# Kernel optimization log

Measured on AMD Instinct MI355X. Metric: run time of the kernel, lower is better.

The kernel has to match this reference:

```python
import jax, jax.numpy as jnp
import numpy as np

B, S, F, E, H, L = 16, 256, 512, 128, 64, 8


def _gru(x, Wih, Whh, bih, bhh):
    """torch-style GRU over time. x: [B,S,E] -> hidden states [B,S,H]."""
    xp = jnp.einsum('bse,ge->bsg', x, Wih) + bih  # [B,S,3H]

    def step(h, xt):
        gh = h @ Whh.T + bhh                      # [B,3H]
        xr, xz, xn = jnp.split(xt, 3, axis=-1)
        hr, hz, hn = jnp.split(gh, 3, axis=-1)
        r = jax.nn.sigmoid(xr + hr)
        z = jax.nn.sigmoid(xz + hz)
        n = jnp.tanh(xn + r * hn)
        h_new = (1.0 - z) * n + z * h
        return h_new, h_new

    h0 = jnp.zeros((x.shape[0], Whh.shape[1]), x.dtype)
    _, hs = jax.lax.scan(step, h0, jnp.swapaxes(xp, 0, 1))  # [S,B,H]
    return jnp.swapaxes(hs, 0, 1)


def setup_inputs() -> dict:
    ks = jax.random.split(jax.random.key(0), 24)
    u = lambda k, shape, n: jax.random.uniform(k, shape, jnp.float32, -1.0 / np.sqrt(n), 1.0 / np.sqrt(n))
    inp = {
        'X': jax.random.normal(ks[0], (B, S, F), jnp.float32),
        'M': jnp.ones((B, S), jnp.float32),
        'cur_M': jax.random.uniform(ks[1], (B, S), jnp.float32),
        # embed linear [E,F]
        'W_embed': u(ks[2], (E, F), F), 'b_embed': u(ks[3], (E,), F),
        # GRU alpha
        'Wih_a': u(ks[4], (3 * H, E), H), 'Whh_a': u(ks[5], (3 * H, H), H),
        'bih_a': u(ks[6], (3 * H,), H), 'bhh_a': u(ks[7], (3 * H,), H),
        # GRU beta
        'Wih_b': u(ks[8], (3 * H, E), H), 'Whh_b': u(ks[9], (3 * H, H), H),
        'bih_b': u(ks[10], (3 * H,), H), 'bhh_b': u(ks[11], (3 * H,), H),
        # attention linears
        'Wb': u(ks[12], (E, H), H), 'bb': u(ks[13], (E,), H),
        'Wa': u(ks[14], (1, H), H), 'ba': u(ks[15], (1,), H),
        # predict linear
        'Wp': u(ks[16], (L, E), E), 'bp': u(ks[17], (L,), E),
    }
    return inp


def reference(X, M, cur_M, W_embed, b_embed,
              Wih_a, Whh_a, bih_a, bhh_a,
              Wih_b, Whh_b, bih_b, bhh_b,
              Wb, bb, Wa, ba, Wp, bp):
    n_seq = X.shape[1]
    emb = jnp.einsum('bsf,ef->bse', X, W_embed) + b_embed          # [B,S,E]
    h_alpha = _gru(emb, Wih_a, Whh_a, bih_a, bhh_a)                # [B,S,H]
    h_beta = _gru(emb, Wih_b, Whh_b, bih_b, bhh_b)                 # [B,S,H]

    # RETAIN attention
    beta_w = jnp.tanh(jnp.einsum('bsh,eh->bse', h_beta, Wb) + bb)  # [B,S,E]
    corr = (jnp.einsum('bsh,oh->bso', h_alpha, Wa) + ba)[..., 0]   # [B,S]
    attn = jnp.exp(corr)                                           # [B,S] (indexed by j)
    flag = jnp.triu(jnp.ones((n_seq, n_seq), X.dtype))             # flag[i,j]=1 iff j>=i
    flag_m = flag[None, :, :] * M[:, None, :]                      # [B,S,S]
    num = attn[:, None, :] * flag_m                                # [B,i,j]
    denom = num.sum(-1, keepdims=True) + 1e-10                     # [B,S,1]
    alpha_w = num / denom                                          # [B,S,S]
    # sum_j alpha[b,i,j] * beta_w[b,j,:] * emb[b,j,:]  (same math as the
    # original broadcasted [B,S,S,E] product, without materializing it)
    weighted = jnp.einsum('bij,bje->bie', alpha_w, beta_w * emb)   # [B,S,E]

    all_output = (jnp.einsum('bse,le->bsl', weighted, Wp) + bp) * M[..., None]  # [B,S,L]
    cur_output = (all_output * cur_M[..., None]).sum(axis=1)                    # [B,L]
    return all_output, cur_output
```

## Files before the change

### kernel.cpp

```cpp
#include <hip/hip_runtime.h>
#include <math.h>

#define BB 16
#define SS 256
#define FF 512
#define EE 128
#define HH 64
#define GG 192
#define LL 8
#define TT 16

__device__ __forceinline__ float sigmoid_f(float x) {
    return 1.0f / (1.0f + __expf(-x));
}
__device__ __forceinline__ float tanh_f(float x) {
    return 1.0f - 2.0f / (1.0f + __expf(2.0f * x));
}

__device__ __forceinline__ void gemm_bt_body(
    const float* __restrict__ A, const float* __restrict__ Bm,
    const float* __restrict__ bias, float* __restrict__ C,
    int N, int K)
{
    __shared__ float As[32][68];
    __shared__ float Bs[64][68];
    const int t = threadIdx.x;
    const int row0 = blockIdx.x * 32;
    const int col0 = blockIdx.y * 64;
    const int tr = t & 7;
    const int tc = t >> 3;
    float acc[4][2] = {{0.f,0.f},{0.f,0.f},{0.f,0.f},{0.f,0.f}};

    for (int k0 = 0; k0 < K; k0 += 64) {
        {
            int r = t >> 3;
            int q = t & 7;
            const float* src = &A[(size_t)(row0 + r) * K + k0];
            #pragma unroll
            for (int it = 0; it < 2; ++it) {
                int kk = (q + it * 8) * 4;
                *(float4*)&As[r][kk] = *(const float4*)&src[kk];
            }
        }
        {
            int r = t >> 2;
            int q = t & 3;
            int n = col0 + r;
            #pragma unroll
            for (int it = 0; it < 4; ++it) {
                int kk = (q + it * 4) * 4;
                float4 v = {0.f, 0.f, 0.f, 0.f};
                if (n < N) v = *(const float4*)&Bm[(size_t)n * K + k0 + kk];
                *(float4*)&Bs[r][kk] = v;
            }
        }
        __syncthreads();
        #pragma unroll
        for (int k = 0; k < 64; k += 4) {
            float4 av[4], bv[2];
            #pragma unroll
            for (int i = 0; i < 4; ++i) av[i] = *(const float4*)&As[tr + 8*i][k];
            #pragma unroll
            for (int j = 0; j < 2; ++j) bv[j] = *(const float4*)&Bs[tc + 32*j][k];
            #pragma unroll
            for (int i = 0; i < 4; ++i)
                #pragma unroll
                for (int j = 0; j < 2; ++j)
                    acc[i][j] += av[i].x*bv[j].x + av[i].y*bv[j].y
                               + av[i].z*bv[j].z + av[i].w*bv[j].w;
        }
        __syncthreads();
    }

    #pragma unroll
    for (int i = 0; i < 4; ++i) {
        int r = row0 + tr + 8*i;
        #pragma unroll
        for (int j = 0; j < 2; ++j) {
            int c = col0 + tc + 32*j;
            if (c < N) C[(size_t)r * N + c] = acc[i][j] + bias[c];
        }
    }
}

__global__ __launch_bounds__(256) void gemm_bt(
    const float* __restrict__ A, const float* __restrict__ Bm,
    const float* __restrict__ bias, float* __restrict__ C,
    int N, int K)
{
    gemm_bt_body(A, Bm, bias, C, N, K);
}

__global__ __launch_bounds__(256) void gemm_bt_dual(
    const float* __restrict__ A,
    const float* __restrict__ B0, const float* __restrict__ bias0, float* __restrict__ C0,
    const float* __restrict__ B1, const float* __restrict__ bias1, float* __restrict__ C1,
    int N, int K)
{
    const float* Bm   = blockIdx.z ? B1    : B0;
    const float* bias = blockIdx.z ? bias1 : bias0;
    float*       C    = blockIdx.z ? C1    : C0;
    gemm_bt_body(A, Bm, bias, C, N, K);
}

__global__ __launch_bounds__(192, 1)
__attribute__((amdgpu_waves_per_eu(1, 1)))
void gru_kernel(
    const float* __restrict__ xpa, const float* __restrict__ xpb,
    const float* __restrict__ Whh_a, const float* __restrict__ bhh_a,
    const float* __restrict__ Whh_b, const float* __restrict__ bhh_b,
    float* __restrict__ hs_a, float* __restrict__ hs_b)
{
    const int blk = blockIdx.x;
    const int b = blk >> 1;
    const int which = blk & 1;
    const float* xp  = which ? xpb   : xpa;
    const float* Whh = which ? Whh_b : Whh_a;
    const float* bhh = which ? bhh_b : bhh_a;
    float* hs        = which ? hs_b  : hs_a;

    const int t = threadIdx.x;
    const int g = t >> 6;
    const int j = t & 63;

    __shared__ float gh_s[2][GG];

    const float4* wrow = (const float4*)&Whh[(size_t)(g * 64 + j) * HH];
    float4 w0  = wrow[0],  w1  = wrow[1],  w2  = wrow[2],  w3  = wrow[3];
    float4 w4  = wrow[4],  w5  = wrow[5],  w6  = wrow[6],  w7  = wrow[7];
    float4 w8  = wrow[8],  w9  = wrow[9],  w10 = wrow[10], w11 = wrow[11];
    float4 w12 = wrow[12], w13 = wrow[13], w14 = wrow[14], w15 = wrow[15];

    const float bh = bhh[g * 64 + j];

    const float* xrow = xp + (size_t)b * SS * GG;
    float* hrow = hs + (size_t)b * SS * HH;
    float hcur = 0.f;

    float xg = xrow[g * 64 + j];
    float xn = xrow[128 + j];

#define RL(v, k) __int_as_float(__builtin_amdgcn_readlane(__float_as_int(v), (k)))
#define DOT4(W, i)                                  \
    a0 = fmaf(W.x, RL(hcur, 4*(i) + 0), a0);        \
    a1 = fmaf(W.y, RL(hcur, 4*(i) + 1), a1);        \
    a2 = fmaf(W.z, RL(hcur, 4*(i) + 2), a2);        \
    a3 = fmaf(W.w, RL(hcur, 4*(i) + 3), a3);

    for (int s = 0; s < SS; ++s) {
        const float* nx = xrow + GG;
        float nxg = nx[g * 64 + j];
        float nxn = nx[128 + j];

        float a0 = bh, a1 = 0.f, a2 = 0.f, a3 = 0.f;
        DOT4(w0, 0)   DOT4(w1, 1)   DOT4(w2, 2)   DOT4(w3, 3)
        DOT4(w4, 4)   DOT4(w5, 5)   DOT4(w6, 6)   DOT4(w7, 7)
        DOT4(w8, 8)   DOT4(w9, 9)   DOT4(w10, 10) DOT4(w11, 11)
        DOT4(w12, 12) DOT4(w13, 13) DOT4(w14, 14) DOT4(w15, 15)
        float pre = (a0 + a1) + (a2 + a3);
        gh_s[s & 1][t] = (g < 2) ? (xg + pre) : pre;

        asm volatile("s_waitcnt lgkmcnt(0)" ::: "memory");
        __builtin_amdgcn_s_barrier();
        asm volatile("" ::: "memory");

        float ghr = gh_s[s & 1][j];
        float ghz = gh_s[s & 1][64 + j];
        float ghn = gh_s[s & 1][128 + j];
        float r = sigmoid_f(ghr);
        float z = sigmoid_f(ghz);
        float n = tanh_f(xn + r * ghn);
        hcur = fmaf(z, hcur - n, n);
        if (g == 0) hrow[j] = hcur;

        xg = nxg; xn = nxn;
        xrow += GG;
        hrow += HH;
    }
#undef DOT4
#undef RL
}

__global__ __launch_bounds__(128) void attn_scanA_kernel(
    const float* __restrict__ h_alpha, const float* __restrict__ h_beta,
    const float* __restrict__ emb, const float* __restrict__ M,
    const float* __restrict__ Wa, const float* __restrict__ ba,
    const float* __restrict__ Wb, const float* __restrict__ bb,
    float* __restrict__ val, float* __restrict__ wj,
    float* __restrict__ tsum, float* __restrict__ wsum)
{
    const int b = blockIdx.x, tt = blockIdx.y;
    const int t = threadIdx.x;
    const int j0 = tt * 16;
    __shared__ float hb_s[HH];
    __shared__ float wj_s;

    const float bbt = bb[t];
    const float4* wrow = (const float4*)&Wb[(size_t)t * HH];

    float ts = 0.f;
    float ws = 0.f;

    for (int jj = 0; jj < 16; ++jj) {
        const int row = b * SS + j0 + jj;
        if (t < 64) {
            hb_s[t] = h_beta[(size_t)row * HH + t];
            float p = h_alpha[(size_t)row * HH + t] * Wa[t];
            #pragma unroll
            for (int off = 32; off > 0; off >>= 1) p += __shfl_down(p, off);
            if (t == 0) {
                float a = __expf(p + ba[0]) * M[row];
                wj_s = a;
                wj[row] = a;
            }
        }
        __syncthreads();

        float acc = bbt;
        #pragma unroll
        for (int k = 0; k < 16; ++k) {
            float4 w4 = wrow[k];
            float4 h4 = *(const float4*)&hb_s[k * 4];
            acc += w4.x*h4.x + w4.y*h4.y + w4.z*h4.z + w4.w*h4.w;
        }
        float v = tanh_f(acc) * emb[(size_t)row * EE + t] * wj_s;
        val[(size_t)row * EE + t] = v;
        ts += v;
        if (t == 0) ws += wj_s;
        __syncthreads();
    }

    tsum[((size_t)(b * TT + tt)) * EE + t] = ts;
    if (t == 0) wsum[b * TT + tt] = ws;
}

__global__ __launch_bounds__(128) void scanB_proj_kernel(
    const float* __restrict__ val, const float* __restrict__ wj,
    const float* __restrict__ tsum, const float* __restrict__ wsum,
    const float* __restrict__ Wp, const float* __restrict__ bp,
    const float* __restrict__ M, float* __restrict__ out)
{
    const int b = blockIdx.x, tt = blockIdx.y;
    const int t = threadIdx.x;
    const int j0 = tt * 16;

    __shared__ float wtd_s[16][132];
    __shared__ float wp_s[8][132];

    float se = 0.f;
    for (int t2 = tt + 1; t2 < TT; ++t2)
        se += tsum[((size_t)(b * TT + t2)) * EE + t];
    float d = 1e-10f;
    for (int t2 = tt + 1; t2 < TT; ++t2)
        d += wsum[b * TT + t2];

    for (int jj = 15; jj >= 0; --jj) {
        size_t idx = ((size_t)(b * SS + j0 + jj)) * EE + t;
        se += val[idx];
        d += wj[b * SS + j0 + jj];
        wtd_s[jj][t] = se / d;
    }

    #pragma unroll
    for (int it = 0; it < 2; ++it) {
        int idx = t + it * 128;
        int r = idx >> 5;
        int c = idx & 31;
        *(float4*)&wp_s[r][c * 4] = *(const float4*)&Wp[(size_t)r * EE + c * 4];
    }
    __syncthreads();

    const int r = t >> 3, l = t & 7;
    float acc = 0.f;
    #pragma unroll
    for (int i = 0; i < 32; ++i) {
        float4 a = *(const float4*)&wtd_s[r][i * 4];
        float4 w = *(const float4*)&wp_s[l][i * 4];
        acc += a.x*w.x + a.y*w.y + a.z*w.z + a.w*w.w;
    }
    const int row = b * SS + j0 + r;
    out[(size_t)row * LL + l] = (acc + bp[l]) * M[row];
}

__global__ __launch_bounds__(256) void cur_kernel(
    const float* __restrict__ out_all, const float* __restrict__ curM,
    float* __restrict__ out_cur)
{
    const int b = blockIdx.x;
    const int t = threadIdx.x;
    const int l = t & 7, c = t >> 3;
    float p = 0.f;
    #pragma unroll
    for (int k = 0; k < 8; ++k) {
        int s = c + k * 32;
        p += out_all[((size_t)(b * SS + s)) * LL + l] * curM[b * SS + s];
    }
    __shared__ float red[32][9];
    red[c][l] = p;
    __syncthreads();
    if (t < 8) {
        float sum = 0.f;
        for (int c2 = 0; c2 < 32; ++c2) sum += red[c2][t];
        out_cur[b * LL + t] = sum;
    }
}

extern "C" void kernel_launch(void* const* d_in, const int* in_sizes, int n_in,
                              void* d_out, int out_size, void* d_ws, size_t ws_size,
                              hipStream_t stream)
{
    const float* X       = (const float*)d_in[0];
    const float* M       = (const float*)d_in[1];
    const float* cur_M   = (const float*)d_in[2];
    const float* W_embed = (const float*)d_in[3];
    const float* b_embed = (const float*)d_in[4];
    const float* Wih_a   = (const float*)d_in[5];
    const float* Whh_a   = (const float*)d_in[6];
    const float* bih_a   = (const float*)d_in[7];
    const float* bhh_a   = (const float*)d_in[8];
    const float* Wih_b   = (const float*)d_in[9];
    const float* Whh_b   = (const float*)d_in[10];
    const float* bih_b   = (const float*)d_in[11];
    const float* bhh_b   = (const float*)d_in[12];
    const float* Wb      = (const float*)d_in[13];
    const float* bb      = (const float*)d_in[14];
    const float* Wa      = (const float*)d_in[15];
    const float* ba      = (const float*)d_in[16];
    const float* Wp      = (const float*)d_in[17];
    const float* bp      = (const float*)d_in[18];
    float* out = (float*)d_out;

    float* ws  = (float*)d_ws;
    float* emb = ws;
    float* xpa = emb + (size_t)BB*SS*EE;
    float* xpb = xpa + (size_t)BB*SS*GG;
    float* ha  = xpb + (size_t)BB*SS*GG;
    float* hb  = ha  + (size_t)BB*SS*HH;
    float* val = hb  + (size_t)BB*SS*HH;
    float* wjv = val + (size_t)BB*SS*EE;
    float* tsum = wjv + (size_t)BB*SS;
    float* wsum = tsum + (size_t)BB*TT*EE;

    const int ROWS = BB * SS;

    gemm_bt<<<dim3(ROWS/32, EE/64), 256, 0, stream>>>(X, W_embed, b_embed, emb, EE, FF);
    gemm_bt_dual<<<dim3(ROWS/32, (GG+63)/64, 2), 256, 0, stream>>>(
        emb, Wih_a, bih_a, xpa, Wih_b, bih_b, xpb, GG, EE);
    gru_kernel<<<32, 192, 0, stream>>>(xpa, xpb, Whh_a, bhh_a, Whh_b, bhh_b, ha, hb);
    attn_scanA_kernel<<<dim3(BB, TT), 128, 0, stream>>>(
        ha, hb, emb, M, Wa, ba, Wb, bb, val, wjv, tsum, wsum);
    scanB_proj_kernel<<<dim3(BB, TT), 128, 0, stream>>>(
        val, wjv, tsum, wsum, Wp, bp, M, out);
    cur_kernel<<<BB, 256, 0, stream>>>(out, cur_M, out + (size_t)BB*SS*LL);
}
```

Baseline: 173.1 us.

## Run GRU recurrence in a single wavefront with packed fp16 dot products

The recurrent weights are converted to packed fp16 by a new pre-kernel. The GRU kernel now uses one 64-lane wavefront per sequence, with each lane computing all three gates for its hidden unit via fdot2 on broadcast fp16 hidden-state pairs. This removes the per-timestep LDS exchange and block barrier across three waves, and halves the readlane count per step. The cost is fp16 rounding of the weights and hidden state inside the dot products, three times more dot work per lane on the serial path, and one extra kernel launch.

Measured after the change: 182.9 us. 1.06x slower.

```diff
diff --git a/kernel.cpp b/kernel.cpp
--- a/kernel.cpp
+++ b/kernel.cpp
@@ -10,6 +10,8 @@
 #define LL 8
 #define TT 16
 
+typedef __fp16 f16x2 __attribute__((ext_vector_type(2)));
+
 __device__ __forceinline__ float sigmoid_f(float x) {
     return 1.0f / (1.0f + __expf(-x));
 }
@@ -103,82 +105,106 @@
     gemm_bt_body(A, Bm, bias, C, N, K);
 }
 
-__global__ __launch_bounds__(192, 1)
+__global__ __launch_bounds__(256) void cvt_w16_kernel(
+    const float* __restrict__ Whh_a, const float* __restrict__ Whh_b,
+    unsigned* __restrict__ wa16, unsigned* __restrict__ wb16)
+{
+    int i = blockIdx.x * 256 + threadIdx.x;
+    if (i < GG * HH / 2) {
+        float2 a = ((const float2*)Whh_a)[i];
+        float2 b = ((const float2*)Whh_b)[i];
+        f16x2 pa = __builtin_amdgcn_cvt_pkrtz(a.x, a.y);
+        f16x2 pb = __builtin_amdgcn_cvt_pkrtz(b.x, b.y);
+        wa16[i] = __builtin_bit_cast(unsigned, pa);
+        wb16[i] = __builtin_bit_cast(unsigned, pb);
+    }
+}
+
+__global__ __launch_bounds__(64, 1)
 __attribute__((amdgpu_waves_per_eu(1, 1)))
 void gru_kernel(
     const float* __restrict__ xpa, const float* __restrict__ xpb,
-    const float* __restrict__ Whh_a, const float* __restrict__ bhh_a,
-    const float* __restrict__ Whh_b, const float* __restrict__ bhh_b,
+    const unsigned* __restrict__ wa16, const unsigned* __restrict__ wb16,
+    const float* __restrict__ bhh_a, const float* __restrict__ bhh_b,
     float* __restrict__ hs_a, float* __restrict__ hs_b)
 {
     const int blk = blockIdx.x;
     const int b = blk >> 1;
     const int which = blk & 1;
-    const float* xp  = which ? xpb   : xpa;
-    const float* Whh = which ? Whh_b : Whh_a;
-    const float* bhh = which ? bhh_b : bhh_a;
-    float* hs        = which ? hs_b  : hs_a;
-
-    const int t = threadIdx.x;
-    const int g = t >> 6;
-    const int j = t & 63;
-
-    __shared__ float gh_s[2][GG];
-
-    const float4* wrow = (const float4*)&Whh[(size_t)(g * 64 + j) * HH];
-    float4 w0  = wrow[0],  w1  = wrow[1],  w2  = wrow[2],  w3  = wrow[3];
-    float4 w4  = wrow[4],  w5  = wrow[5],  w6  = wrow[6],  w7  = wrow[7];
-    float4 w8  = wrow[8],  w9  = wrow[9],  w10 = wrow[10], w11 = wrow[11];
-    float4 w12 = wrow[12], w13 = wrow[13], w14 = wrow[14], w15 = wrow[15];
-
-    const float bh = bhh[g * 64 + j];
+    const float* xp    = which ? xpb  : xpa;
+    const unsigned* wf = which ? wb16 : wa16;
+    const float* bhh   = which ? bhh_b : bhh_a;
+    float* hs          = which ? hs_b  : hs_a;
+
+    const int j = threadIdx.x;
+
+    const uint4* pr = (const uint4*)(wf + (size_t)j * 32);
+    const uint4* pz = (const uint4*)(wf + (size_t)(j + 64) * 32);
+    const uint4* pn = (const uint4*)(wf + (size_t)(j + 128) * 32);
+    uint4 r0 = pr[0], r1 = pr[1], r2 = pr[2], r3 = pr[3];
+    uint4 r4 = pr[4], r5 = pr[5], r6 = pr[6], r7 = pr[7];
+    uint4 z0 = pz[0], z1 = pz[1], z2 = pz[2], z3 = pz[3];
+    uint4 z4 = pz[4], z5 = pz[5], z6 = pz[6], z7 = pz[7];
+    uint4 n0 = pn[0], n1 = pn[1], n2 = pn[2], n3 = pn[3];
+    uint4 n4 = pn[4], n5 = pn[5], n6 = pn[6], n7 = pn[7];
+
+    const float br = bhh[j], bz = bhh[j + 64], bn = bhh[j + 128];
 
     const float* xrow = xp + (size_t)b * SS * GG;
     float* hrow = hs + (size_t)b * SS * HH;
     float hcur = 0.f;
 
-    float xg = xrow[g * 64 + j];
-    float xn = xrow[128 + j];
-
-#define RL(v, k) __int_as_float(__builtin_amdgcn_readlane(__float_as_int(v), (k)))
-#define DOT4(W, i)                                  \
-    a0 = fmaf(W.x, RL(hcur, 4*(i) + 0), a0);        \
-    a1 = fmaf(W.y, RL(hcur, 4*(i) + 1), a1);        \
-    a2 = fmaf(W.z, RL(hcur, 4*(i) + 2), a2);        \
-    a3 = fmaf(W.w, RL(hcur, 4*(i) + 3), a3);
+    float xr = xrow[j], xz = xrow[j + 64], xn = xrow[j + 128];
+
+#define BCH(u) __builtin_bit_cast(f16x2, (unsigned)(u))
+#define RLH(k) ((unsigned)__builtin_amdgcn_readlane(__builtin_bit_cast(int, hp), (k)))
+#define FD(W, H, A) A = __builtin_amdgcn_fdot2(BCH(W), H, A, false)
+#define QUAD(q)                                                \
+    {                                                          \
+        f16x2 h0_ = BCH(RLH(8*(q) + 0));                       \
+        f16x2 h1_ = BCH(RLH(8*(q) + 2));                       \
+        f16x2 h2_ = BCH(RLH(8*(q) + 4));                       \
+        f16x2 h3_ = BCH(RLH(8*(q) + 6));                       \
+        FD(r##q.x, h0_, ar0); FD(r##q.y, h1_, ar1);            \
+        FD(r##q.z, h2_, ar2); FD(r##q.w, h3_, ar3);            \
+        FD(z##q.x, h0_, az0); FD(z##q.y, h1_, az1);            \
+        FD(z##q.z, h2_, az2); FD(z##q.w, h3_, az3);            \
+        FD(n##q.x, h0_, an0); FD(n##q.y, h1_, an1);            \
+        FD(n##q.z, h2_, an2); FD(n##q.w, h3_, an3);            \
+    }
 
     for (int s = 0; s < SS; ++s) {
         const float* nx = xrow + GG;
-        float nxg = nx[g * 64 + j];
-        float nxn = nx[128 + j];
-
-        float a0 = bh, a1 = 0.f, a2 = 0.f, a3 = 0.f;
-        DOT4(w0, 0)   DOT4(w1, 1)   DOT4(w2, 2)   DOT4(w3, 3)
-        DOT4(w4, 4)   DOT4(w5, 5)   DOT4(w6, 6)   DOT4(w7, 7)
-        DOT4(w8, 8)   DOT4(w9, 9)   DOT4(w10, 10) DOT4(w11, 11)
-        DOT4(w12, 12) DOT4(w13, 13) DOT4(w14, 14) DOT4(w15, 15)
-        float pre = (a0 + a1) + (a2 + a3);
-        gh_s[s & 1][t] = (g < 2) ? (xg + pre) : pre;
-
-        asm volatile("s_waitcnt lgkmcnt(0)" ::: "memory");
-        __builtin_amdgcn_s_barrier();
-        asm volatile("" ::: "memory");
-
-        float ghr = gh_s[s & 1][j];
-        float ghz = gh_s[s & 1][64 + j];
-        float ghn = gh_s[s & 1][128 + j];
-        float r = sigmoid_f(ghr);
-        float z = sigmoid_f(ghz);
-        float n = tanh_f(xn + r * ghn);
+        float nxr = nx[j], nxz = nx[j + 64], nxn = nx[128 + j];
+
+        float partner = __shfl_xor(hcur, 1);
+        float ev = (j & 1) ? partner : hcur;
+        float od = (j & 1) ? hcur : partner;
+        f16x2 hp = __builtin_amdgcn_cvt_pkrtz(ev, od);
+
+        float ar0 = br, ar1 = 0.f, ar2 = 0.f, ar3 = 0.f;
+        float az0 = bz, az1 = 0.f, az2 = 0.f, az3 = 0.f;
+        float an0 = bn, an1 = 0.f, an2 = 0.f, an3 = 0.f;
+        QUAD(0) QUAD(1) QUAD(2) QUAD(3)
+        QUAD(4) QUAD(5) QUAD(6) QUAD(7)
+        float arr = (ar0 + ar1) + (ar2 + ar3);
+        float azz = (az0 + az1) + (az2 + az3);
+        float ann = (an0 + an1) + (an2 + an3);
+
+        float r = sigmoid_f(xr + arr);
+        float z = sigmoid_f(xz + azz);
+        float n = tanh_f(xn + r * ann);
         hcur = fmaf(z, hcur - n, n);
-        if (g == 0) hrow[j] = hcur;
-
-        xg = nxg; xn = nxn;
+        hrow[j] = hcur;
+
+        xr = nxr; xz = nxz; xn = nxn;
         xrow += GG;
         hrow += HH;
     }
-#undef DOT4
-#undef RL
+#undef QUAD
+#undef FD
+#undef RLH
+#undef BCH
 }
 
 __global__ __launch_bounds__(128) void attn_scanA_kernel(
@@ -340,13 +366,16 @@
     float* wjv = val + (size_t)BB*SS*EE;
     float* tsum = wjv + (size_t)BB*SS;
     float* wsum = tsum + (size_t)BB*TT*EE;
+    unsigned* wa16 = (unsigned*)(wsum + (size_t)BB*TT);
+    unsigned* wb16 = wa16 + (size_t)GG*HH/2;
 
     const int ROWS = BB * SS;
 
+    cvt_w16_kernel<<<24, 256, 0, stream>>>(Whh_a, Whh_b, wa16, wb16);
     gemm_bt<<<dim3(ROWS/32, EE/64), 256, 0, stream>>>(X, W_embed, b_embed, emb, EE, FF);
     gemm_bt_dual<<<dim3(ROWS/32, (GG+63)/64, 2), 256, 0, stream>>>(
         emb, Wih_a, bih_a, xpa, Wih_b, bih_b, xpb, GG, EE);
-    gru_kernel<<<32, 192, 0, stream>>>(xpa, xpb, Whh_a, bhh_a, Whh_b, bhh_b, ha, hb);
+    gru_kernel<<<32, 64, 0, stream>>>(xpa, xpb, wa16, wb16, bhh_a, bhh_b, ha, hb);
     attn_scanA_kernel<<<dim3(BB, TT), 128, 0, stream>>>(
         ha, hb, emb, M, Wa, ba, Wb, bb, val, wjv, tsum, wsum);
     scanB_proj_kernel<<<dim3(BB, TT), 128, 0, stream>>>(
```

## Pack two GRU chains per block and fuse cur reduction into projection

Applied to the files above, without the earlier changes.

The GRU kernel now runs two independent recurrences (alpha and beta for one batch) in a single 384-thread block sharing one barrier, halving the block count from 32 to 16. The separate cur_kernel is removed. Its weighted sum over time is folded into scanB_proj_kernel through a shared-memory partial sum and an atomicAdd, with the output zeroed by a memset first. This cuts one launch but adds atomics and a memset. Coupling two chains on one barrier lets them wait on each other, and the waves_per_eu hint is dropped.

Result: slower. 249.3 us (+44.0%).

```diff
diff --git a/kernel.cpp b/kernel.cpp
--- a/kernel.cpp
+++ b/kernel.cpp
@@ -103,27 +103,28 @@
     gemm_bt_body(A, Bm, bias, C, N, K);
 }
 
-__global__ __launch_bounds__(192, 1)
-__attribute__((amdgpu_waves_per_eu(1, 1)))
+__global__ __launch_bounds__(384, 1)
 void gru_kernel(
     const float* __restrict__ xpa, const float* __restrict__ xpb,
     const float* __restrict__ Whh_a, const float* __restrict__ bhh_a,
     const float* __restrict__ Whh_b, const float* __restrict__ bhh_b,
     float* __restrict__ hs_a, float* __restrict__ hs_b)
 {
-    const int blk = blockIdx.x;
-    const int b = blk >> 1;
-    const int which = blk & 1;
+    const int t = threadIdx.x;
+    const int c = (t >= 192) ? 1 : 0;
+    const int tc = t - c * 192;
+    const int g = tc >> 6;
+    const int j = tc & 63;
+
+    const int chain = blockIdx.x * 2 + c;
+    const int b = chain >> 1;
+    const int which = chain & 1;
     const float* xp  = which ? xpb   : xpa;
     const float* Whh = which ? Whh_b : Whh_a;
     const float* bhh = which ? bhh_b : bhh_a;
     float* hs        = which ? hs_b  : hs_a;
 
-    const int t = threadIdx.x;
-    const int g = t >> 6;
-    const int j = t & 63;
-
-    __shared__ float gh_s[2][GG];
+    __shared__ float gh_s[2][2][GG];
 
     const float4* wrow = (const float4*)&Whh[(size_t)(g * 64 + j) * HH];
     float4 w0  = wrow[0],  w1  = wrow[1],  w2  = wrow[2],  w3  = wrow[3];
@@ -158,15 +159,15 @@
         DOT4(w8, 8)   DOT4(w9, 9)   DOT4(w10, 10) DOT4(w11, 11)
         DOT4(w12, 12) DOT4(w13, 13) DOT4(w14, 14) DOT4(w15, 15)
         float pre = (a0 + a1) + (a2 + a3);
-        gh_s[s & 1][t] = (g < 2) ? (xg + pre) : pre;
+        gh_s[s & 1][c][tc] = (g < 2) ? (xg + pre) : pre;
 
         asm volatile("s_waitcnt lgkmcnt(0)" ::: "memory");
         __builtin_amdgcn_s_barrier();
         asm volatile("" ::: "memory");
 
-        float ghr = gh_s[s & 1][j];
-        float ghz = gh_s[s & 1][64 + j];
-        float ghn = gh_s[s & 1][128 + j];
+        float ghr = gh_s[s & 1][c][j];
+        float ghz = gh_s[s & 1][c][64 + j];
+        float ghn = gh_s[s & 1][c][128 + j];
         float r = sigmoid_f(ghr);
         float z = sigmoid_f(ghz);
         float n = tanh_f(xn + r * ghn);
@@ -238,7 +239,8 @@
     const float* __restrict__ val, const float* __restrict__ wj,
     const float* __restrict__ tsum, const float* __restrict__ wsum,
     const float* __restrict__ Wp, const float* __restrict__ bp,
-    const float* __restrict__ M, float* __restrict__ out)
+    const float* __restrict__ M, const float* __restrict__ curM,
+    float* __restrict__ out, float* __restrict__ out_cur)
 {
     const int b = blockIdx.x, tt = blockIdx.y;
     const int t = threadIdx.x;
@@ -246,6 +248,7 @@
 
     __shared__ float wtd_s[16][132];
     __shared__ float wp_s[8][132];
+    __shared__ float red_s[16][8];
 
     float se = 0.f;
     for (int t2 = tt + 1; t2 < TT; ++t2)
@@ -279,29 +282,16 @@
         acc += a.x*w.x + a.y*w.y + a.z*w.z + a.w*w.w;
     }
     const int row = b * SS + j0 + r;
-    out[(size_t)row * LL + l] = (acc + bp[l]) * M[row];
-}
-
-__global__ __launch_bounds__(256) void cur_kernel(
-    const float* __restrict__ out_all, const float* __restrict__ curM,
-    float* __restrict__ out_cur)
-{
-    const int b = blockIdx.x;
-    const int t = threadIdx.x;
-    const int l = t & 7, c = t >> 3;
-    float p = 0.f;
-    #pragma unroll
-    for (int k = 0; k < 8; ++k) {
-        int s = c + k * 32;
-        p += out_all[((size_t)(b * SS + s)) * LL + l] * curM[b * SS + s];
-    }
-    __shared__ float red[32][9];
-    red[c][l] = p;
+    float ov = (acc + bp[l]) * M[row];
+    out[(size_t)row * LL + l] = ov;
+
+    red_s[r][l] = ov * curM[row];
     __syncthreads();
     if (t < 8) {
         float sum = 0.f;
-        for (int c2 = 0; c2 < 32; ++c2) sum += red[c2][t];
-        out_cur[b * LL + t] = sum;
+        #pragma unroll
+        for (int r2 = 0; r2 < 16; ++r2) sum += red_s[r2][t];
+        atomicAdd(&out_cur[b * LL + t], sum);
     }
 }
 
@@ -329,6 +319,7 @@
     const float* Wp      = (const float*)d_in[17];
     const float* bp      = (const float*)d_in[18];
     float* out = (float*)d_out;
+    float* out_cur = out + (size_t)BB * SS * LL;
 
     float* ws  = (float*)d_ws;
     float* emb = ws;
@@ -343,13 +334,13 @@
 
     const int ROWS = BB * SS;
 
+    hipMemsetAsync(out_cur, 0, (size_t)BB * LL * sizeof(float), stream);
     gemm_bt<<<dim3(ROWS/32, EE/64), 256, 0, stream>>>(X, W_embed, b_embed, emb, EE, FF);
     gemm_bt_dual<<<dim3(ROWS/32, (GG+63)/64, 2), 256, 0, stream>>>(
         emb, Wih_a, bih_a, xpa, Wih_b, bih_b, xpb, GG, EE);
-    gru_kernel<<<32, 192, 0, stream>>>(xpa, xpb, Whh_a, bhh_a, Whh_b, bhh_b, ha, hb);
+    gru_kernel<<<16, 384, 0, stream>>>(xpa, xpb, Whh_a, bhh_a, Whh_b, bhh_b, ha, hb);
     attn_scanA_kernel<<<dim3(BB, TT), 128, 0, stream>>>(
         ha, hb, emb, M, Wa, ba, Wb, bb, val, wjv, tsum, wsum);
     scanB_proj_kernel<<<dim3(BB, TT), 128, 0, stream>>>(
-        val, wjv, tsum, wsum, Wp, bp, M, out);
-    cur_kernel<<<BB, 256, 0, stream>>>(out, cur_M, out + (size_t)BB*SS*LL);
-}
+        val, wjv, tsum, wsum, Wp, bp, M, cur_M, out, out_cur);
+}
```
